# Kernel tuning notes

Measured on AMD Instinct MI355X. Metric: run time of the kernel, lower is better.

## Reference

```python
import jax, jax.numpy as jnp
import numpy as np

B, P, G = 32, 8000, 100
IMG = 800.0
HIGH_T, LOW_T = 0.5, 0.5          # torchvision Matcher thresholds for RoI heads
BATCH_PER_IMG, POS_FRAC = 512, 0.25
W_X, W_Y, W_W, W_H = 10.0, 10.0, 5.0, 5.0  # BoxCoder weights


def _rand_boxes(key, shape):
    k1, k2 = jax.random.split(key)
    xy = jax.random.uniform(k1, shape + (2,), minval=0.0, maxval=IMG - 200.0)
    wh = jax.random.uniform(k2, shape + (2,), minval=8.0, maxval=200.0)
    return jnp.concatenate([xy, xy + wh], axis=-1)  # valid xyxy boxes


def setup_inputs() -> dict:
    key = jax.random.key(0)
    kp, kg, kl = jax.random.split(key, 3)
    return {
        "proposals": _rand_boxes(kp, (B, P)),        # [B, P, 4]
        "gt_boxes": _rand_boxes(kg, (B, G)),         # [B, G, 4]
        "gt_labels": jax.random.randint(kl, (B, G), 1, 14),  # [B, G], classes 1..13
    }


def _box_iou(gt, pr):
    # gt [B,G,4], pr [B,Pt,4] -> [B,G,Pt]
    area_g = (gt[..., 2] - gt[..., 0]) * (gt[..., 3] - gt[..., 1])
    area_p = (pr[..., 2] - pr[..., 0]) * (pr[..., 3] - pr[..., 1])
    lt = jnp.maximum(gt[:, :, None, :2], pr[:, None, :, :2])
    rb = jnp.minimum(gt[:, :, None, 2:], pr[:, None, :, 2:])
    wh = jnp.clip(rb - lt, 0.0)
    inter = wh[..., 0] * wh[..., 1]
    return inter / (area_g[:, :, None] + area_p[:, None, :] - inter)


def _rank_desc(score):
    # rank of each element if sorted descending, per row
    order = jnp.argsort(-score, axis=1)
    return jnp.argsort(order, axis=1)


def _encode(ref_gt, prop):
    # BoxCoder.encode with weights (10,10,5,5)
    pw = prop[..., 2] - prop[..., 0]
    ph = prop[..., 3] - prop[..., 1]
    px = prop[..., 0] + 0.5 * pw
    py = prop[..., 1] + 0.5 * ph
    gw = ref_gt[..., 2] - ref_gt[..., 0]
    gh = ref_gt[..., 3] - ref_gt[..., 1]
    gx = ref_gt[..., 0] + 0.5 * gw
    gy = ref_gt[..., 1] + 0.5 * gh
    return jnp.stack([W_X * (gx - px) / pw,
                      W_Y * (gy - py) / ph,
                      W_W * jnp.log(gw / pw),
                      W_H * jnp.log(gh / ph)], axis=-1)


def reference(proposals, gt_boxes, gt_labels):
    # select_training_samples: add_gt_proposals -> match -> label -> subsample -> encode
    props = jnp.concatenate([proposals, gt_boxes], axis=1)      # [B, P+G, 4]
    iou = _box_iou(gt_boxes, props)                             # [B, G, P+G]
    vals = iou.max(axis=1)
    midx = iou.argmax(axis=1)
    # Matcher: below low -> -1 (bg), between -> -2 (ignore)
    matched = jnp.where(vals < LOW_T, -1, jnp.where(vals < HIGH_T, -2, midx))
    clamped = jnp.clip(matched, 0)
    labels = jnp.take_along_axis(gt_labels, clamped, axis=1)
    labels = jnp.where(matched == -1, 0, labels)
    labels = jnp.where(matched == -2, -1, labels)
    # BalancedPositiveNegativeSampler(512, 0.25): random subset, fixed total
    r = jax.random.uniform(jax.random.key(42), labels.shape)
    pos = labels >= 1
    neg = labels == 0
    n_pos_cap = int(BATCH_PER_IMG * POS_FRAC)
    sel_pos = pos & (_rank_desc(jnp.where(pos, r, -1.0)) < n_pos_cap)
    n_pos = sel_pos.sum(axis=1, keepdims=True)
    sel_neg = neg & (_rank_desc(jnp.where(neg, r, -1.0)) < (BATCH_PER_IMG - n_pos))
    selected = sel_pos | sel_neg
    # emulate torch.nonzero ordering: selected indices in ascending index order
    Pt = props.shape[1]
    prio = selected.astype(jnp.float32) * (2.0 * Pt) - jnp.arange(Pt, dtype=jnp.float32)
    _, sampled_inds = jax.lax.top_k(prio, BATCH_PER_IMG)        # [B, 512]
    s_props = jnp.take_along_axis(props, sampled_inds[..., None], axis=1)
    s_labels = jnp.take_along_axis(labels, sampled_inds, axis=1)
    s_midx = jnp.take_along_axis(clamped, sampled_inds, axis=1)
    matched_gt = jnp.take_along_axis(gt_boxes, s_midx[..., None], axis=1)
    reg_targets = _encode(matched_gt, s_props)                  # [B, 512, 4]
    return s_props, s_labels, reg_targets
```

## Files before the change

### kernel.cpp

```cpp
#include <hip/hip_runtime.h>

#define BB 32
#define PP 8000
#define GG 100
#define PT 8100
#define NSEL 512
#define POSCAP 128
#define OFF_LAB 65536
#define OFF_REG 81920
#define NT1 256
#define NT2 1024
#define NW2 (NT2 / 64)
#define SPAN 512
#define HB 4096
#define GCAP 512

__device__ __forceinline__ unsigned rotl32(unsigned x, int r) {
  return (x << r) | (x >> (32 - r));
}

__device__ __forceinline__ unsigned threefry_bits(unsigned ctr) {
  const unsigned k0 = 0u, k1 = 42u;
  const unsigned k2 = k0 ^ k1 ^ 0x1BD11BDAu;
  unsigned x0 = 0u + k0;
  unsigned x1 = ctr + k1;
#define TF4(a,b,c,d) \
  x0 += x1; x1 = rotl32(x1,(a)); x1 ^= x0; \
  x0 += x1; x1 = rotl32(x1,(b)); x1 ^= x0; \
  x0 += x1; x1 = rotl32(x1,(c)); x1 ^= x0; \
  x0 += x1; x1 = rotl32(x1,(d)); x1 ^= x0;
  TF4(13,15,26, 6)  x0 += k1; x1 += k2 + 1u;
  TF4(17,29,16,24)  x0 += k2; x1 += k0 + 2u;
  TF4(13,15,26, 6)  x0 += k0; x1 += k1 + 3u;
  TF4(17,29,16,24)  x0 += k1; x1 += k2 + 4u;
  TF4(13,15,26, 6)  x0 += k2; x1 += k0 + 5u;
#undef TF4
  return x0 ^ x1;
}

__global__ __launch_bounds__(NT1) void label_kernel(
    const float* __restrict__ proposals,
    const float* __restrict__ gt_boxes,
    const int*   __restrict__ gt_labels,
    unsigned*    __restrict__ packed,
    unsigned char* __restrict__ midxv)
{
  const int b = blockIdx.y;
  const int t = blockIdx.x * NT1 + threadIdx.x;

  __shared__ float sgx[GG], sgy[GG], sgX[GG], sgY[GG], sarea[GG];
  __shared__ int   slab[GG];
  if (threadIdx.x < GG) {
    int g = threadIdx.x;
    float4 q = ((const float4*)gt_boxes)[(size_t)b * GG + g];
    sgx[g] = q.x; sgy[g] = q.y; sgX[g] = q.z; sgY[g] = q.w;
    sarea[g] = (q.z - q.x) * (q.w - q.y);
    slab[g] = gt_labels[b * GG + g];
  }
  __syncthreads();
  if (t >= PT) return;

  float4 p = (t < PP) ? ((const float4*)proposals)[(size_t)b * PP + t]
                      : ((const float4*)gt_boxes)[(size_t)b * GG + (t - PP)];
  float area_p = (p.z - p.x) * (p.w - p.y);
  asm volatile("" : "+v"(area_p));

  float best = -1.0f;
  int bidx = 0;
  for (int g = 0; g < GG; ++g) {
    float w = fminf(sgX[g], p.z) - fmaxf(sgx[g], p.x);
    float h = fminf(sgY[g], p.w) - fmaxf(sgy[g], p.y);
    w = fmaxf(w, 0.0f);
    h = fmaxf(h, 0.0f);
    float inter = w * h;
    asm volatile("" : "+v"(inter));
    float uni = (sarea[g] + area_p) - inter;
    float iou = inter / uni;
    if (iou > best) { best = iou; bidx = g; }
  }

  int cls, m;
  if (best < 0.5f) { cls = 0; m = 0; }
  else             { cls = slab[bidx]; m = bidx; }

  unsigned bits = threefry_bits((unsigned)(b * PT + t));
  packed[(size_t)b * PT + t] = (bits >> 9) | ((unsigned)cls << 24);
  midxv[(size_t)b * PT + t] = (unsigned char)m;
}

__global__ __launch_bounds__(NT2) void select_kernel(
    const float*    __restrict__ proposals,
    const float*    __restrict__ gt_boxes,
    const unsigned* __restrict__ packed,
    const unsigned char* __restrict__ midxv,
    float* __restrict__ out)
{
  const int b = blockIdx.x;
  const int tid = threadIdx.x;
  const int lane = tid & 63;
  const int wid = tid >> 6;
  const unsigned long long laneLT = (lane == 63) ? 0x7FFFFFFFFFFFFFFFull
                                                 : ((1ull << lane) - 1ull);

  __shared__ unsigned sp[PT];
  __shared__ unsigned hist[HB];
  __shared__ unsigned waveTot[NW2];
  __shared__ unsigned wHard[NW2], wTP[NW2], wTN[NW2];
  __shared__ unsigned gbufP[GCAP], gbufN[GCAP];
  __shared__ unsigned sBin[2], sAbove[2], sTheta[2], sM[2], sCnt[2];

  for (int t = tid; t < PT; t += NT2) sp[t] = packed[(size_t)b * PT + t];
#pragma unroll
  for (int i = 0; i < HB / NT2; ++i) hist[tid + i * NT2] = 0u;
  __syncthreads();

  for (int t = tid; t < PT; t += NT2) {
    unsigned v = sp[t];
    unsigned bin = (v & 0x7FFFFFu) >> 11;
    atomicAdd(&hist[bin], (v >> 24) >= 1u ? 1u : 0x10000u);
  }
  __syncthreads();

  const int BPT = HB / NT2;
  unsigned local = 0;
#pragma unroll
  for (int j = 0; j < BPT; ++j) local += hist[tid * BPT + j];
  unsigned suf = local;
  for (int d = 1; d < 64; d <<= 1) {
    unsigned o = __shfl_down(suf, d, 64);
    if (lane + d < 64) suf += o;
  }
  if (lane == 0) waveTot[wid] = suf;
  __syncthreads();

  unsigned totAll = 0, waveAfter = 0;
#pragma unroll
  for (int w = 0; w < NW2; ++w) { unsigned x = waveTot[w]; totAll += x; if (w > wid) waveAfter += x; }
  unsigned num_pos = totAll & 0xFFFFu, num_neg = totAll >> 16;
  bool allP = (num_pos <= POSCAP);
  unsigned capP = allP ? num_pos : POSCAP;
  unsigned Kneg = NSEL - capP;
  bool allN = (num_neg <= Kneg);
  unsigned sumAfter = waveAfter + (suf - local);
  {
    unsigned aP = sumAfter & 0xFFFFu, aN = sumAfter >> 16;
#pragma unroll
    for (int j = BPT - 1; j >= 0; --j) {
      unsigned hc = hist[tid * BPT + j];
      unsigned hp = hc & 0xFFFFu, hn = hc >> 16;
      if (!allP && aP < POSCAP && aP + hp >= POSCAP) { sBin[0] = tid * BPT + j; sAbove[0] = aP; }
      if (!allN && aN < Kneg   && aN + hn >= Kneg)   { sBin[1] = tid * BPT + j; sAbove[1] = aN; }
      aP += hp; aN += hn;
    }
  }
  if (tid < 2) sCnt[tid] = 0u;
  __syncthreads();

  unsigned binP = sBin[0], binN = sBin[1];
  for (int t = tid; t < PT; t += NT2) {
    unsigned v = sp[t];
    unsigned key = v & 0x7FFFFFu;
    bool isP = (v >> 24) >= 1u;
    if (!allP && isP && (key >> 11) == binP) {
      unsigned i = atomicAdd(&sCnt[0], 1u);
      if (i < GCAP) gbufP[i] = key;
    }
    if (!allN && !isP && (key >> 11) == binN) {
      unsigned i = atomicAdd(&sCnt[1], 1u);
      if (i < GCAP) gbufN[i] = key;
    }
  }
  __syncthreads();

  if (wid == 0 && !allP) {
    int n = min((int)sCnt[0], GCAP);
    unsigned above = sAbove[0];
    unsigned r = POSCAP - above;
    for (int i = lane; i < n; i += 64) {
      unsigned ki = gbufP[i];
      unsigned gt = 0, ge = 0;
      for (int j = 0; j < n; ++j) { unsigned kj = gbufP[j]; gt += (kj > ki); ge += (kj >= ki); }
      if (gt < r && ge >= r) { sTheta[0] = ki; sM[0] = POSCAP - (above + gt); }
    }
  }
  if (wid == 1 && !allN) {
    int n = min((int)sCnt[1], GCAP);
    unsigned above = sAbove[1];
    unsigned r = Kneg - above;
    for (int i = lane; i < n; i += 64) {
      unsigned ki = gbufN[i];
      unsigned gt = 0, ge = 0;
      for (int j = 0; j < n; ++j) { unsigned kj = gbufN[j]; gt += (kj > ki); ge += (kj >= ki); }
      if (gt < r && ge >= r) { sTheta[1] = ki; sM[1] = Kneg - (above + gt); }
    }
  }
  __syncthreads();

  unsigned thetaP = allP ? 0u : sTheta[0];
  unsigned mP     = allP ? 0u : sM[0];
  unsigned thetaN = allN ? 0u : sTheta[1];
  unsigned mN     = allN ? 0u : sM[1];

  const int s0 = wid * SPAN;
  unsigned hardCnt = 0, tpCnt = 0, tnCnt = 0;
#pragma unroll
  for (int step = 0; step < SPAN / 64; ++step) {
    int t = s0 + step * 64 + lane;
    bool hard = false, tp = false, tn = false;
    if (t < PT) {
      unsigned v = sp[t];
      unsigned key = v & 0x7FFFFFu;
      if ((v >> 24) >= 1u) {
        if (allP || key > thetaP) hard = true;
        else if (key == thetaP)   tp = true;
      } else {
        if (allN || key > thetaN) hard = true;
        else if (key == thetaN)   tn = true;
      }
    }
    hardCnt += __popcll(__ballot(hard));
    tpCnt   += __popcll(__ballot(tp));
    tnCnt   += __popcll(__ballot(tn));
  }
  if (lane == 0) { wHard[wid] = hardCnt; wTP[wid] = tpCnt; wTN[wid] = tnCnt; }
  __syncthreads();

  unsigned tieBaseP = 0, tieBaseN = 0, posBase = 0;
  {
    unsigned tb = 0, nb = 0;
#pragma unroll
    for (int w = 0; w < NW2; ++w) {
      if (w == wid) { tieBaseP = tb; tieBaseN = nb; break; }
      unsigned takeP = (mP > tb) ? min(mP - tb, wTP[w]) : 0u;
      unsigned takeN = (mN > nb) ? min(mN - nb, wTN[w]) : 0u;
      posBase += wHard[w] + takeP + takeN;
      tb += wTP[w]; nb += wTN[w];
    }
  }

  unsigned runP = tieBaseP, runN = tieBaseN, posRun = posBase;
#pragma unroll
  for (int step = 0; step < SPAN / 64; ++step) {
    int t = s0 + step * 64 + lane;
    bool hard = false, tp = false, tn = false;
    unsigned cls = 0;
    if (t < PT) {
      unsigned v = sp[t];
      unsigned key = v & 0x7FFFFFu;
      cls = v >> 24;
      if (cls >= 1u) {
        if (allP || key > thetaP) hard = true;
        else if (key == thetaP)   tp = true;
      } else {
        if (allN || key > thetaN) hard = true;
        else if (key == thetaN)   tn = true;
      }
    }
    unsigned long long mtp = __ballot(tp);
    unsigned long long mtn = __ballot(tn);
    bool sel = hard
             | (tp && (runP + __popcll(mtp & laneLT)) < mP)
             | (tn && (runN + __popcll(mtn & laneLT)) < mN);
    unsigned long long msel = __ballot(sel);

    if (sel) {
      unsigned pos = posRun + __popcll(msel & laneLT);
      float4 p = (t < PP) ? ((const float4*)proposals)[(size_t)b * PP + t]
                          : ((const float4*)gt_boxes)[(size_t)b * GG + (t - PP)];
      int m = midxv[(size_t)b * PT + t];
      float4 gq = ((const float4*)gt_boxes)[(size_t)b * GG + m];

      size_t o1 = (size_t)b * NSEL + pos;
      out[o1 * 4 + 0] = p.x;
      out[o1 * 4 + 1] = p.y;
      out[o1 * 4 + 2] = p.z;
      out[o1 * 4 + 3] = p.w;
      out[OFF_LAB + o1] = (float)cls;

      float pw = p.z - p.x, ph = p.w - p.y;
      float px = p.x + 0.5f * pw, py = p.y + 0.5f * ph;
      float gw = gq.z - gq.x, gh = gq.w - gq.y;
      float gx = gq.x + 0.5f * gw, gy = gq.y + 0.5f * gh;
      size_t o2 = OFF_REG + o1 * 4;
      out[o2 + 0] = 10.0f * (gx - px) / pw;
      out[o2 + 1] = 10.0f * (gy - py) / ph;
      out[o2 + 2] = 5.0f * logf(gw / pw);
      out[o2 + 3] = 5.0f * logf(gh / ph);
    }

    runP += __popcll(mtp);
    runN += __popcll(mtn);
    posRun += __popcll(msel);
  }
}

extern "C" void kernel_launch(void* const* d_in, const int* in_sizes, int n_in,
                              void* d_out, int out_size, void* d_ws, size_t ws_size,
                              hipStream_t stream) {
  const float* proposals = (const float*)d_in[0];
  const float* gt_boxes  = (const float*)d_in[1];
  const int*   gt_labels = (const int*)d_in[2];
  float* out = (float*)d_out;

  unsigned* packed = (unsigned*)d_ws;
  unsigned char* midxv = (unsigned char*)d_ws + (size_t)BB * PT * sizeof(unsigned);

  dim3 g1((PT + NT1 - 1) / NT1, BB);
  label_kernel<<<g1, NT1, 0, stream>>>(proposals, gt_boxes, gt_labels, packed, midxv);
  select_kernel<<<BB, NT2, 0, stream>>>(proposals, gt_boxes, packed, midxv, out);
}
```

Baseline: 45.54 us.

## Fuse label and select kernels into one cooperative launch with grid sync

Merges the IoU labeling kernel and the per-image selection kernel into a single cooperative kernel of 256 blocks of 1024 threads. A grid-wide sync separates the two phases, and then only the first 32 blocks carry on with selection. This removes the second launch and the gap between kernels. It also loads the packed array as uint4 with the histogram fused into that load, and reads GT boxes as float4 from shared memory. The cost is the grid-sync overhead, larger blocks in the labeling phase, and a dependence on all 256 blocks being co-resident.

```diff
diff --git a/kernel.cpp b/kernel.cpp
--- a/kernel.cpp
+++ b/kernel.cpp
@@ -1,19 +1,23 @@
 #include <hip/hip_runtime.h>
+#include <hip/hip_cooperative_groups.h>
+
+namespace cg = cooperative_groups;
 
 #define BB 32
 #define PP 8000
 #define GG 100
 #define PT 8100
+#define PT4 2025
 #define NSEL 512
 #define POSCAP 128
 #define OFF_LAB 65536
 #define OFF_REG 81920
-#define NT1 256
-#define NT2 1024
-#define NW2 (NT2 / 64)
+#define NTHR 1024
+#define NWAVE 16
 #define SPAN 512
 #define HB 4096
 #define GCAP 512
+#define NBLK 256
 
 __device__ __forceinline__ unsigned rotl32(unsigned x, int r) {
   return (x << r) | (x >> (32 - r));
@@ -38,90 +42,96 @@
   return x0 ^ x1;
 }
 
-__global__ __launch_bounds__(NT1) void label_kernel(
+__global__ __launch_bounds__(NTHR) void roiheads_coop(
     const float* __restrict__ proposals,
     const float* __restrict__ gt_boxes,
     const int*   __restrict__ gt_labels,
     unsigned*    __restrict__ packed,
-    unsigned char* __restrict__ midxv)
+    unsigned char* __restrict__ midxv,
+    float*       __restrict__ out)
 {
-  const int b = blockIdx.y;
-  const int t = blockIdx.x * NT1 + threadIdx.x;
-
-  __shared__ float sgx[GG], sgy[GG], sgX[GG], sgY[GG], sarea[GG];
-  __shared__ int   slab[GG];
-  if (threadIdx.x < GG) {
-    int g = threadIdx.x;
-    float4 q = ((const float4*)gt_boxes)[(size_t)b * GG + g];
-    sgx[g] = q.x; sgy[g] = q.y; sgX[g] = q.z; sgY[g] = q.w;
-    sarea[g] = (q.z - q.x) * (q.w - q.y);
-    slab[g] = gt_labels[b * GG + g];
-  }
-  __syncthreads();
-  if (t >= PT) return;
-
-  float4 p = (t < PP) ? ((const float4*)proposals)[(size_t)b * PP + t]
-                      : ((const float4*)gt_boxes)[(size_t)b * GG + (t - PP)];
-  float area_p = (p.z - p.x) * (p.w - p.y);
-  asm volatile("" : "+v"(area_p));
-
-  float best = -1.0f;
-  int bidx = 0;
-  for (int g = 0; g < GG; ++g) {
-    float w = fminf(sgX[g], p.z) - fmaxf(sgx[g], p.x);
-    float h = fminf(sgY[g], p.w) - fmaxf(sgy[g], p.y);
-    w = fmaxf(w, 0.0f);
-    h = fmaxf(h, 0.0f);
-    float inter = w * h;
-    asm volatile("" : "+v"(inter));
-    float uni = (sarea[g] + area_p) - inter;
-    float iou = inter / uni;
-    if (iou > best) { best = iou; bidx = g; }
-  }
-
-  int cls, m;
-  if (best < 0.5f) { cls = 0; m = 0; }
-  else             { cls = slab[bidx]; m = bidx; }
-
-  unsigned bits = threefry_bits((unsigned)(b * PT + t));
-  packed[(size_t)b * PT + t] = (bits >> 9) | ((unsigned)cls << 24);
-  midxv[(size_t)b * PT + t] = (unsigned char)m;
-}
-
-__global__ __launch_bounds__(NT2) void select_kernel(
-    const float*    __restrict__ proposals,
-    const float*    __restrict__ gt_boxes,
-    const unsigned* __restrict__ packed,
-    const unsigned char* __restrict__ midxv,
-    float* __restrict__ out)
-{
-  const int b = blockIdx.x;
   const int tid = threadIdx.x;
   const int lane = tid & 63;
   const int wid = tid >> 6;
+
+  __shared__ float4  sgq[GG];
+  __shared__ float   sarea[GG];
+  __shared__ int     slab[GG];
+  __shared__ __align__(16) unsigned sp[PT];
+  __shared__ unsigned hist[HB];
+  __shared__ unsigned waveTot[NWAVE];
+  __shared__ unsigned wHard[NWAVE], wTP[NWAVE], wTN[NWAVE];
+  __shared__ unsigned gbufP[GCAP], gbufN[GCAP];
+  __shared__ unsigned sBin[2], sAbove[2], sTheta[2], sM[2], sCnt[2];
+
+  {
+    const int b = blockIdx.x >> 3;
+    const int c = blockIdx.x & 7;
+    if (tid < GG) {
+      float4 q = ((const float4*)gt_boxes)[(size_t)b * GG + tid];
+      sgq[tid] = q;
+      sarea[tid] = (q.z - q.x) * (q.w - q.y);
+      slab[tid] = gt_labels[b * GG + tid];
+    }
+    __syncthreads();
+
+    const int t = c * NTHR + tid;
+    if (t < PT) {
+      float4 p = (t < PP) ? ((const float4*)proposals)[(size_t)b * PP + t]
+                          : ((const float4*)gt_boxes)[(size_t)b * GG + (t - PP)];
+      float area_p = (p.z - p.x) * (p.w - p.y);
+      asm volatile("" : "+v"(area_p));
+
+      float best = -1.0f;
+      int bidx = 0;
+      for (int g = 0; g < GG; ++g) {
+        float4 q = sgq[g];
+        float w = fminf(q.z, p.z) - fmaxf(q.x, p.x);
+        float h = fminf(q.w, p.w) - fmaxf(q.y, p.y);
+        w = fmaxf(w, 0.0f);
+        h = fmaxf(h, 0.0f);
+        float inter = w * h;
+        asm volatile("" : "+v"(inter));
+        float uni = (sarea[g] + area_p) - inter;
+        float iou = inter / uni;
+        if (iou > best) { best = iou; bidx = g; }
+      }
+
+      int cls, m;
+      if (best < 0.5f) { cls = 0; m = 0; }
+      else             { cls = slab[bidx]; m = bidx; }
+
+      unsigned bits = threefry_bits((unsigned)(b * PT + t));
+      packed[(size_t)b * PT + t] = (bits >> 9) | ((unsigned)cls << 24);
+      midxv[(size_t)b * PT + t] = (unsigned char)m;
+    }
+  }
+
+  __threadfence();
+  cg::this_grid().sync();
+  if (blockIdx.x >= BB) return;
+
+  const int b = blockIdx.x;
   const unsigned long long laneLT = (lane == 63) ? 0x7FFFFFFFFFFFFFFFull
                                                  : ((1ull << lane) - 1ull);
 
-  __shared__ unsigned sp[PT];
-  __shared__ unsigned hist[HB];
-  __shared__ unsigned waveTot[NW2];
-  __shared__ unsigned wHard[NW2], wTP[NW2], wTN[NW2];
-  __shared__ unsigned gbufP[GCAP], gbufN[GCAP];
-  __shared__ unsigned sBin[2], sAbove[2], sTheta[2], sM[2], sCnt[2];
-
-  for (int t = tid; t < PT; t += NT2) sp[t] = packed[(size_t)b * PT + t];
-#pragma unroll
-  for (int i = 0; i < HB / NT2; ++i) hist[tid + i * NT2] = 0u;
-  __syncthreads();
-
-  for (int t = tid; t < PT; t += NT2) {
-    unsigned v = sp[t];
-    unsigned bin = (v & 0x7FFFFFu) >> 11;
-    atomicAdd(&hist[bin], (v >> 24) >= 1u ? 1u : 0x10000u);
-  }
-  __syncthreads();
-
-  const int BPT = HB / NT2;
+#pragma unroll
+  for (int i = 0; i < HB / NTHR; ++i) hist[tid + i * NTHR] = 0u;
+  __syncthreads();
+
+  {
+    const uint4* pk4 = (const uint4*)(packed + (size_t)b * PT);
+    for (int i = tid; i < PT4; i += NTHR) {
+      uint4 v = pk4[i];
+      ((uint4*)sp)[i] = v;
+#define H1(x) atomicAdd(&hist[((x) & 0x7FFFFFu) >> 11], ((x) >> 24) >= 1u ? 1u : 0x10000u)
+      H1(v.x); H1(v.y); H1(v.z); H1(v.w);
+#undef H1
+    }
+  }
+  __syncthreads();
+
+  const int BPT = HB / NTHR;
   unsigned local = 0;
 #pragma unroll
   for (int j = 0; j < BPT; ++j) local += hist[tid * BPT + j];
@@ -135,7 +145,7 @@
 
   unsigned totAll = 0, waveAfter = 0;
 #pragma unroll
-  for (int w = 0; w < NW2; ++w) { unsigned x = waveTot[w]; totAll += x; if (w > wid) waveAfter += x; }
+  for (int w = 0; w < NWAVE; ++w) { unsigned x = waveTot[w]; totAll += x; if (w > wid) waveAfter += x; }
   unsigned num_pos = totAll & 0xFFFFu, num_neg = totAll >> 16;
   bool allP = (num_pos <= POSCAP);
   unsigned capP = allP ? num_pos : POSCAP;
@@ -157,7 +167,7 @@
   __syncthreads();
 
   unsigned binP = sBin[0], binN = sBin[1];
-  for (int t = tid; t < PT; t += NT2) {
+  for (int t = tid; t < PT; t += NTHR) {
     unsigned v = sp[t];
     unsigned key = v & 0x7FFFFFu;
     bool isP = (v >> 24) >= 1u;
@@ -229,7 +239,7 @@
   {
     unsigned tb = 0, nb = 0;
 #pragma unroll
-    for (int w = 0; w < NW2; ++w) {
+    for (int w = 0; w < NWAVE; ++w) {
       if (w == wid) { tieBaseP = tb; tieBaseN = nb; break; }
       unsigned takeP = (mP > tb) ? min(mP - tb, wTP[w]) : 0u;
       unsigned takeN = (mN > nb) ? min(mN - nb, wTN[w]) : 0u;
@@ -305,7 +315,8 @@
   unsigned* packed = (unsigned*)d_ws;
   unsigned char* midxv = (unsigned char*)d_ws + (size_t)BB * PT * sizeof(unsigned);
 
-  dim3 g1((PT + NT1 - 1) / NT1, BB);
-  label_kernel<<<g1, NT1, 0, stream>>>(proposals, gt_boxes, gt_labels, packed, midxv);
-  select_kernel<<<BB, NT2, 0, stream>>>(proposals, gt_boxes, packed, midxv, out);
+  void* args[6] = { (void*)&proposals, (void*)&gt_boxes, (void*)&gt_labels,
+                    (void*)&packed, (void*)&midxv, (void*)&out };
+  hipLaunchCooperativeKernel((const void*)roiheads_coop, dim3(NBLK), dim3(NTHR),
+                             args, 0, stream);
 }
```

New measurement: 162.5 us. 3.57x slower.

## Keep packed keys in registers with lane-contiguous ownership instead of LDS staging

Applied to the files above, without the earlier changes.

Each thread loads 8 contiguous packed keys with two vectorized 16-byte loads and keeps them in registers for the whole select kernel. This removes the shared-memory copy of the whole row and its repeated re-reads in the histogram, gather, count and emit phases. Because each lane now owns a contiguous chunk, the in-wave ordering and tie-break prefix sums are rebuilt from per-element ballots plus per-lane running prefixes. The cost is more registers and less coalesced per-lane gathers and output stores. The vector loads for the last wave also read past the end of each row.

```diff
diff --git a/kernel.cpp b/kernel.cpp
--- a/kernel.cpp
+++ b/kernel.cpp
@@ -10,8 +10,9 @@
 #define OFF_REG 81920
 #define NT1 256
 #define NT2 1024
-#define NW2 (NT2 / 64)
+#define NWAVE 16
 #define SPAN 512
+#define KPL 8
 #define HB 4096
 #define GCAP 512
 
@@ -99,25 +100,34 @@
   const int tid = threadIdx.x;
   const int lane = tid & 63;
   const int wid = tid >> 6;
-  const unsigned long long laneLT = (lane == 63) ? 0x7FFFFFFFFFFFFFFFull
-                                                 : ((1ull << lane) - 1ull);
-
-  __shared__ unsigned sp[PT];
+  const unsigned long long laneLT = (1ull << lane) - 1ull;
+
   __shared__ unsigned hist[HB];
-  __shared__ unsigned waveTot[NW2];
-  __shared__ unsigned wHard[NW2], wTP[NW2], wTN[NW2];
+  __shared__ unsigned waveTot[NWAVE];
+  __shared__ unsigned wHard[NWAVE], wTP[NWAVE], wTN[NWAVE];
   __shared__ unsigned gbufP[GCAP], gbufN[GCAP];
   __shared__ unsigned sBin[2], sAbove[2], sTheta[2], sM[2], sCnt[2];
 
-  for (int t = tid; t < PT; t += NT2) sp[t] = packed[(size_t)b * PT + t];
+  const int s0 = wid * SPAN;
+  const int tBase = s0 + lane * KPL;
+  unsigned k[KPL];
+  {
+    const uint4* pk4 = (const uint4*)(packed + (size_t)b * PT);
+    uint4 va = pk4[(s0 >> 2) + lane * 2];
+    uint4 vb = pk4[(s0 >> 2) + lane * 2 + 1];
+    k[0]=va.x; k[1]=va.y; k[2]=va.z; k[3]=va.w;
+    k[4]=vb.x; k[5]=vb.y; k[6]=vb.z; k[7]=vb.w;
+  }
+
 #pragma unroll
   for (int i = 0; i < HB / NT2; ++i) hist[tid + i * NT2] = 0u;
   __syncthreads();
 
-  for (int t = tid; t < PT; t += NT2) {
-    unsigned v = sp[t];
-    unsigned bin = (v & 0x7FFFFFu) >> 11;
-    atomicAdd(&hist[bin], (v >> 24) >= 1u ? 1u : 0x10000u);
+#pragma unroll
+  for (int j = 0; j < KPL; ++j) {
+    if (tBase + j < PT)
+      atomicAdd(&hist[(k[j] & 0x7FFFFFu) >> 11],
+                (k[j] >> 24) >= 1u ? 1u : 0x10000u);
   }
   __syncthreads();
 
@@ -131,11 +141,12 @@
     if (lane + d < 64) suf += o;
   }
   if (lane == 0) waveTot[wid] = suf;
+  if (tid < 2) sCnt[tid] = 0u;
   __syncthreads();
 
   unsigned totAll = 0, waveAfter = 0;
 #pragma unroll
-  for (int w = 0; w < NW2; ++w) { unsigned x = waveTot[w]; totAll += x; if (w > wid) waveAfter += x; }
+  for (int w = 0; w < NWAVE; ++w) { unsigned x = waveTot[w]; totAll += x; if (w > wid) waveAfter += x; }
   unsigned num_pos = totAll & 0xFFFFu, num_neg = totAll >> 16;
   bool allP = (num_pos <= POSCAP);
   unsigned capP = allP ? num_pos : POSCAP;
@@ -153,21 +164,22 @@
       aP += hp; aN += hn;
     }
   }
-  if (tid < 2) sCnt[tid] = 0u;
   __syncthreads();
 
   unsigned binP = sBin[0], binN = sBin[1];
-  for (int t = tid; t < PT; t += NT2) {
-    unsigned v = sp[t];
-    unsigned key = v & 0x7FFFFFu;
-    bool isP = (v >> 24) >= 1u;
-    if (!allP && isP && (key >> 11) == binP) {
-      unsigned i = atomicAdd(&sCnt[0], 1u);
-      if (i < GCAP) gbufP[i] = key;
-    }
-    if (!allN && !isP && (key >> 11) == binN) {
-      unsigned i = atomicAdd(&sCnt[1], 1u);
-      if (i < GCAP) gbufN[i] = key;
+#pragma unroll
+  for (int j = 0; j < KPL; ++j) {
+    if (tBase + j < PT) {
+      unsigned key = k[j] & 0x7FFFFFu;
+      bool isP = (k[j] >> 24) >= 1u;
+      if (!allP && isP && (key >> 11) == binP) {
+        unsigned i = atomicAdd(&sCnt[0], 1u);
+        if (i < GCAP) gbufP[i] = key;
+      }
+      if (!allN && !isP && (key >> 11) == binN) {
+        unsigned i = atomicAdd(&sCnt[1], 1u);
+        if (i < GCAP) gbufN[i] = key;
+      }
     }
   }
   __syncthreads();
@@ -201,26 +213,26 @@
   unsigned thetaN = allN ? 0u : sTheta[1];
   unsigned mN     = allN ? 0u : sM[1];
 
-  const int s0 = wid * SPAN;
+  unsigned myHard = 0, myTP = 0, myTN = 0;
+#pragma unroll
+  for (int j = 0; j < KPL; ++j) {
+    if (tBase + j < PT) {
+      unsigned key = k[j] & 0x7FFFFFu;
+      if ((k[j] >> 24) >= 1u) {
+        if (allP || key > thetaP) myHard |= 1u << j;
+        else if (key == thetaP)   myTP |= 1u << j;
+      } else {
+        if (allN || key > thetaN) myHard |= 1u << j;
+        else if (key == thetaN)   myTN |= 1u << j;
+      }
+    }
+  }
   unsigned hardCnt = 0, tpCnt = 0, tnCnt = 0;
 #pragma unroll
-  for (int step = 0; step < SPAN / 64; ++step) {
-    int t = s0 + step * 64 + lane;
-    bool hard = false, tp = false, tn = false;
-    if (t < PT) {
-      unsigned v = sp[t];
-      unsigned key = v & 0x7FFFFFu;
-      if ((v >> 24) >= 1u) {
-        if (allP || key > thetaP) hard = true;
-        else if (key == thetaP)   tp = true;
-      } else {
-        if (allN || key > thetaN) hard = true;
-        else if (key == thetaN)   tn = true;
-      }
-    }
-    hardCnt += __popcll(__ballot(hard));
-    tpCnt   += __popcll(__ballot(tp));
-    tnCnt   += __popcll(__ballot(tn));
+  for (int j = 0; j < KPL; ++j) {
+    hardCnt += __popcll(__ballot((myHard >> j) & 1u));
+    tpCnt   += __popcll(__ballot((myTP   >> j) & 1u));
+    tnCnt   += __popcll(__ballot((myTN   >> j) & 1u));
   }
   if (lane == 0) { wHard[wid] = hardCnt; wTP[wid] = tpCnt; wTN[wid] = tnCnt; }
   __syncthreads();
@@ -229,7 +241,7 @@
   {
     unsigned tb = 0, nb = 0;
 #pragma unroll
-    for (int w = 0; w < NW2; ++w) {
+    for (int w = 0; w < NWAVE; ++w) {
       if (w == wid) { tieBaseP = tb; tieBaseN = nb; break; }
       unsigned takeP = (mP > tb) ? min(mP - tb, wTP[w]) : 0u;
       unsigned takeN = (mN > nb) ? min(mN - nb, wTN[w]) : 0u;
@@ -238,59 +250,64 @@
     }
   }
 
-  unsigned runP = tieBaseP, runN = tieBaseN, posRun = posBase;
-#pragma unroll
-  for (int step = 0; step < SPAN / 64; ++step) {
-    int t = s0 + step * 64 + lane;
-    bool hard = false, tp = false, tn = false;
-    unsigned cls = 0;
-    if (t < PT) {
-      unsigned v = sp[t];
-      unsigned key = v & 0x7FFFFFu;
-      cls = v >> 24;
-      if (cls >= 1u) {
-        if (allP || key > thetaP) hard = true;
-        else if (key == thetaP)   tp = true;
-      } else {
-        if (allN || key > thetaN) hard = true;
-        else if (key == thetaN)   tn = true;
+  {
+    unsigned long long mtp[KPL], mtn[KPL];
+#pragma unroll
+    for (int j = 0; j < KPL; ++j) {
+      mtp[j] = __ballot((myTP >> j) & 1u);
+      mtn[j] = __ballot((myTN >> j) & 1u);
+    }
+    unsigned basTP = tieBaseP, basTN = tieBaseN;
+#pragma unroll
+    for (int j = 0; j < KPL; ++j) {
+      basTP += __popcll(mtp[j] & laneLT);
+      basTN += __popcll(mtn[j] & laneLT);
+    }
+    unsigned mySel = 0, prefTP = 0, prefTN = 0;
+#pragma unroll
+    for (int j = 0; j < KPL; ++j) {
+      bool s = (myHard >> j) & 1u;
+      if ((myTP >> j) & 1u) { s = (basTP + prefTP) < mP; prefTP++; }
+      if ((myTN >> j) & 1u) { s = (basTN + prefTN) < mN; prefTN++; }
+      if (s) mySel |= 1u << j;
+    }
+    unsigned posAcc = posBase;
+#pragma unroll
+    for (int j = 0; j < KPL; ++j)
+      posAcc += __popcll(__ballot((mySel >> j) & 1u) & laneLT);
+
+    unsigned prefSel = 0;
+#pragma unroll
+    for (int j = 0; j < KPL; ++j) {
+      if ((mySel >> j) & 1u) {
+        int t = tBase + j;
+        unsigned cls = k[j] >> 24;
+        unsigned pos = posAcc + prefSel;
+        prefSel++;
+
+        float4 p = (t < PP) ? ((const float4*)proposals)[(size_t)b * PP + t]
+                            : ((const float4*)gt_boxes)[(size_t)b * GG + (t - PP)];
+        int m = midxv[(size_t)b * PT + t];
+        float4 gq = ((const float4*)gt_boxes)[(size_t)b * GG + m];
+
+        size_t o1 = (size_t)b * NSEL + pos;
+        out[o1 * 4 + 0] = p.x;
+        out[o1 * 4 + 1] = p.y;
+        out[o1 * 4 + 2] = p.z;
+        out[o1 * 4 + 3] = p.w;
+        out[OFF_LAB + o1] = (float)cls;
+
+        float pw = p.z - p.x, ph = p.w - p.y;
+        float px = p.x + 0.5f * pw, py = p.y + 0.5f * ph;
+        float gw = gq.z - gq.x, gh = gq.w - gq.y;
+        float gx = gq.x + 0.5f * gw, gy = gq.y + 0.5f * gh;
+        size_t o2 = OFF_REG + o1 * 4;
+        out[o2 + 0] = 10.0f * (gx - px) / pw;
+        out[o2 + 1] = 10.0f * (gy - py) / ph;
+        out[o2 + 2] = 5.0f * logf(gw / pw);
+        out[o2 + 3] = 5.0f * logf(gh / ph);
       }
     }
-    unsigned long long mtp = __ballot(tp);
-    unsigned long long mtn = __ballot(tn);
-    bool sel = hard
-             | (tp && (runP + __popcll(mtp & laneLT)) < mP)
-             | (tn && (runN + __popcll(mtn & laneLT)) < mN);
-    unsigned long long msel = __ballot(sel);
-
-    if (sel) {
-      unsigned pos = posRun + __popcll(msel & laneLT);
-      float4 p = (t < PP) ? ((const float4*)proposals)[(size_t)b * PP + t]
-                          : ((const float4*)gt_boxes)[(size_t)b * GG + (t - PP)];
-      int m = midxv[(size_t)b * PT + t];
-      float4 gq = ((const float4*)gt_boxes)[(size_t)b * GG + m];
-
-      size_t o1 = (size_t)b * NSEL + pos;
-      out[o1 * 4 + 0] = p.x;
-      out[o1 * 4 + 1] = p.y;
-      out[o1 * 4 + 2] = p.z;
-      out[o1 * 4 + 3] = p.w;
-      out[OFF_LAB + o1] = (float)cls;
-
-      float pw = p.z - p.x, ph = p.w - p.y;
-      float px = p.x + 0.5f * pw, py = p.y + 0.5f * ph;
-      float gw = gq.z - gq.x, gh = gq.w - gq.y;
-      float gx = gq.x + 0.5f * gw, gy = gq.y + 0.5f * gh;
-      size_t o2 = OFF_REG + o1 * 4;
-      out[o2 + 0] = 10.0f * (gx - px) / pw;
-      out[o2 + 1] = 10.0f * (gy - py) / ph;
-      out[o2 + 2] = 5.0f * logf(gw / pw);
-      out[o2 + 3] = 5.0f * logf(gh / ph);
-    }
-
-    runP += __popcll(mtp);
-    runN += __popcll(mtn);
-    posRun += __popcll(msel);
   }
 }
 
```

New measurement: 45.89 us. About the same (+0.8%).
